# Performance work log

Hardware: AMD Instinct MI355X
Metric: run time of the kernel (lower is better)

The kernel has to match this reference:

```python
import jax, jax.numpy as jnp
import numpy as np

INV_TEMP = 100.0


def setup_inputs() -> dict:
    key = jax.random.key(0)
    k1, k2, k3 = jax.random.split(key, 3)
    B, C, J, Hh, Wh = 64, 4, 17, 96, 96
    heatmaps = jax.random.normal(k1, (B * C, J, Hh, Wh), dtype=jnp.float32)
    projection_matrices = jax.random.normal(k2, (B, C, 3, 4), dtype=jnp.float32)
    confidences = jax.random.uniform(k3, (B, C, J), dtype=jnp.float32)
    return {
        "heatmaps": heatmaps,
        "projection_matrices": projection_matrices,
        "confidences": confidences,
        "H_img": 384,
        "W_img": 384,
    }


def _softargmax(heatmaps):
    # heatmaps: (B*C, J, Hh, Wh) -> keypoints (B*C, J, 2) as (x, y)
    bc, J, Hh, Wh = heatmaps.shape
    hm = jax.nn.softmax((heatmaps * INV_TEMP).reshape(bc, J, Hh * Wh), axis=-1)
    hm = hm.reshape(bc, J, Hh, Wh)
    xs = jnp.arange(Wh, dtype=hm.dtype)
    ys = jnp.arange(Hh, dtype=hm.dtype)
    kx = jnp.einsum('bjhw,w->bj', hm, xs)  # x = width index (grid c=0)
    ky = jnp.einsum('bjhw,h->bj', hm, ys)  # y = height index (grid c=1)
    return jnp.stack([kx, ky], axis=-1)


def _dlt(P, kp2d, conf):
    # P: (B,C,3,4), kp2d: (B,C,J,2), conf: (B,C,J) -> (B,J,3)
    B, C, J = kp2d.shape[:3]
    # A[b,c,j,i,:] = P[b,c,2,:]*kp2d[b,c,j,i] - P[b,c,i,:], scaled by conf
    A = (P[:, :, None, 2:3, :] * kp2d[:, :, :, :, None]
         - P[:, :, None, :2, :]) * conf[:, :, :, None, None]  # (B,C,J,2,4)
    A = A.transpose(0, 2, 1, 3, 4).reshape(B, J, 2 * C, 4)
    _, _, Vh = jnp.linalg.svd(A, full_matrices=False)  # Vh: (B,J,4,4)
    homo = Vh[..., 3, :]  # smallest right singular vector, (B,J,4)
    return homo[..., :3] / homo[..., 3:4]


def reference(heatmaps, projection_matrices, confidences, H_img, W_img):
    B, C = projection_matrices.shape[:2]
    bc, J, Hh, Wh = heatmaps.shape
    kp = _softargmax(heatmaps)  # (B*C, J, 2)
    # faithful (quirky) rescale: x *= H/Hh, y *= W/Wh as in original code
    scale = jnp.array([H_img / Hh, W_img / Wh], dtype=kp.dtype)
    kp = (kp * scale).reshape(B, C, J, 2)
    return _dlt(projection_matrices, kp, confidences)
```

## Files before the change

kernel.cpp:

```cpp
#include <hip/hip_runtime.h>

#define B_NUM 64
#define C_NUM 4
#define J_NUM 17
#define HH 96
#define WW 96
#define HWSZ (HH * WW)

__device__ __forceinline__ float waveMax(float v) {
#pragma unroll
  for (int o = 32; o > 0; o >>= 1) v = fmaxf(v, __shfl_xor(v, o));
  return v;
}
__device__ __forceinline__ float waveSum(float v) {
#pragma unroll
  for (int o = 32; o > 0; o >>= 1) v += __shfl_xor(v, o);
  return v;
}

__global__ __launch_bounds__(256, 1) void triang_fused_k(
    const float* __restrict__ hm, const float* __restrict__ P,
    const float* __restrict__ conf, const int* __restrict__ Hp,
    const int* __restrict__ Wp, float* __restrict__ out) {
  const int bj = blockIdx.x;
  const int b = bj / J_NUM;
  const int j = bj - b * J_NUM;
  const int t = threadIdx.x;
  const int cam = t >> 6;
  const int lane = t & 63;
  const int r = (b * C_NUM + cam) * J_NUM + j;
  const float4* row = (const float4*)(hm + (size_t)r * HWSZ);

  float4 v[36];
  float m = -3.4e38f;
#pragma unroll
  for (int k = 0; k < 36; ++k) {
    v[k] = row[k * 64 + lane];
    m = fmaxf(m, fmaxf(fmaxf(v[k].x, v[k].y), fmaxf(v[k].z, v[k].w)));
  }
  m = waveMax(m);
  const float M100 = 100.0f * m;

  float se = 0.f, sx = 0.f, sy = 0.f;
#pragma unroll
  for (int k = 0; k < 36; ++k) {
    const int base = k * 256 + lane * 4;
    const float e0 = __expf(fmaf(100.f, v[k].x, -M100));
    const float e1 = __expf(fmaf(100.f, v[k].y, -M100));
    const float e2 = __expf(fmaf(100.f, v[k].z, -M100));
    const float e3 = __expf(fmaf(100.f, v[k].w, -M100));
    const int h = base / WW;
    const int w0 = base - h * WW;
    const float esum = (e0 + e1) + (e2 + e3);
    se += esum;
    sy += esum * (float)h;
    sx += e0 * (float)w0 + e1 * (float)(w0 + 1) + e2 * (float)(w0 + 2) +
          e3 * (float)(w0 + 3);
  }
  se = waveSum(se);
  sx = waveSum(sx);
  sy = waveSum(sy);

  __shared__ float skp[C_NUM][2];
  if (lane == 0) {
    const float scx = (float)Hp[0] / (float)HH;
    const float scy = (float)Wp[0] / (float)WW;
    skp[cam][0] = sx / se * scx;
    skp[cam][1] = sy / se * scy;
  }
  __syncthreads();
  if (t != 0) return;

  double M4[4][4];
#pragma unroll
  for (int a = 0; a < 4; ++a)
#pragma unroll
    for (int bb = 0; bb < 4; ++bb) M4[a][bb] = 0.0;

#pragma unroll
  for (int c = 0; c < C_NUM; ++c) {
    const float* Pm = P + ((size_t)(b * C_NUM + c)) * 12;
    const float cf = conf[(b * C_NUM + c) * J_NUM + j];
    const double x = (double)skp[c][0];
    const double y = (double)skp[c][1];
    double row0[4], row1[4];
#pragma unroll
    for (int l = 0; l < 4; ++l) {
      const double p2 = (double)Pm[8 + l];
      row0[l] = (p2 * x - (double)Pm[l]) * (double)cf;
      row1[l] = (p2 * y - (double)Pm[4 + l]) * (double)cf;
    }
#pragma unroll
    for (int a = 0; a < 4; ++a)
#pragma unroll
      for (int bb = 0; bb < 4; ++bb)
        M4[a][bb] += row0[a] * row0[bb] + row1[a] * row1[bb];
  }

  double V[4][4];
#pragma unroll
  for (int a = 0; a < 4; ++a)
#pragma unroll
    for (int bb = 0; bb < 4; ++bb) V[a][bb] = (a == bb) ? 1.0 : 0.0;

  for (int sweep = 0; sweep < 8; ++sweep) {
#pragma unroll
    for (int p = 0; p < 3; ++p) {
#pragma unroll
      for (int q = p + 1; q < 4; ++q) {
        const double d = M4[p][q];
        if (fabs(d) < 1e-300) continue;
        const double a = M4[p][p], bq = M4[q][q];
        const double theta = (bq - a) / (2.0 * d);
        const double tt = (theta >= 0.0 ? 1.0 : -1.0) /
                          (fabs(theta) + sqrt(theta * theta + 1.0));
        const double cc = 1.0 / sqrt(tt * tt + 1.0);
        const double ss = tt * cc;
#pragma unroll
        for (int k = 0; k < 4; ++k) {
          if (k == p || k == q) continue;
          const double mkp = M4[k][p], mkq = M4[k][q];
          M4[k][p] = M4[p][k] = cc * mkp - ss * mkq;
          M4[k][q] = M4[q][k] = ss * mkp + cc * mkq;
        }
        M4[p][p] = a - tt * d;
        M4[q][q] = bq + tt * d;
        M4[p][q] = M4[q][p] = 0.0;
#pragma unroll
        for (int k = 0; k < 4; ++k) {
          const double vkp = V[k][p], vkq = V[k][q];
          V[k][p] = cc * vkp - ss * vkq;
          V[k][q] = ss * vkp + cc * vkq;
        }
      }
    }
  }

  int mi = 0;
  double mv = M4[0][0];
#pragma unroll
  for (int i = 1; i < 4; ++i)
    if (M4[i][i] < mv) { mv = M4[i][i]; mi = i; }
  const double h3 = V[3][mi];
  out[bj * 3 + 0] = (float)(V[0][mi] / h3);
  out[bj * 3 + 1] = (float)(V[1][mi] / h3);
  out[bj * 3 + 2] = (float)(V[2][mi] / h3);
}

extern "C" void kernel_launch(void* const* d_in, const int* in_sizes, int n_in,
                              void* d_out, int out_size, void* d_ws, size_t ws_size,
                              hipStream_t stream) {
  const float* hm = (const float*)d_in[0];
  const float* P = (const float*)d_in[1];
  const float* conf = (const float*)d_in[2];
  const int* Hp = (const int*)d_in[3];
  const int* Wp = (const int*)d_in[4];
  float* out = (float*)d_out;

  triang_fused_k<<<B_NUM * J_NUM, 256, 0, stream>>>(hm, P, conf, Hp, Wp, out);
}
```

Before: 260.9 us.

## Stream heatmap rows with online softmax and double-buffered nontemporal loads

Replaces the load-everything-then-reduce scheme (36 float4 registers per thread) with four chunks of nine float4 loads. The next chunk is prefetched while the current one is reduced with an online max/rescale softmax. This is meant to cut register pressure so occupancy can rise beyond one block, now that the min-blocks launch bound is dropped. It also overlaps loads with exp math, uses nontemporal loads, and uses exp2 with a folded constant. The cost is extra rescale exps per chunk and one extra cross-lane rescale before the wave sums.

```diff
diff --git a/kernel.cpp b/kernel.cpp
--- a/kernel.cpp
+++ b/kernel.cpp
@@ -6,6 +6,9 @@
 #define HH 96
 #define WW 96
 #define HWSZ (HH * WW)
+#define K100 144.26950408889634f
+
+typedef float f32x4 __attribute__((ext_vector_type(4)));
 
 __device__ __forceinline__ float waveMax(float v) {
 #pragma unroll
@@ -18,48 +21,63 @@
   return v;
 }
 
-__global__ __launch_bounds__(256, 1) void triang_fused_k(
+__global__ __launch_bounds__(256) void triang_k(
     const float* __restrict__ hm, const float* __restrict__ P,
     const float* __restrict__ conf, const int* __restrict__ Hp,
     const int* __restrict__ Wp, float* __restrict__ out) {
   const int bj = blockIdx.x;
   const int b = bj / J_NUM;
   const int j = bj - b * J_NUM;
-  const int t = threadIdx.x;
-  const int cam = t >> 6;
-  const int lane = t & 63;
+  const int cam = threadIdx.x >> 6;
+  const int lane = threadIdx.x & 63;
   const int r = (b * C_NUM + cam) * J_NUM + j;
-  const float4* row = (const float4*)(hm + (size_t)r * HWSZ);
+  const f32x4* row = (const f32x4*)(hm + (size_t)r * HWSZ);
 
-  float4 v[36];
-  float m = -3.4e38f;
+  float m = -3.4e38f, se = 0.f, sx = 0.f, sy = 0.f;
+  f32x4 cur[9], nxt[9];
 #pragma unroll
-  for (int k = 0; k < 36; ++k) {
-    v[k] = row[k * 64 + lane];
-    m = fmaxf(m, fmaxf(fmaxf(v[k].x, v[k].y), fmaxf(v[k].z, v[k].w)));
+  for (int i = 0; i < 9; ++i)
+    cur[i] = __builtin_nontemporal_load(row + i * 64 + lane);
+
+#pragma unroll
+  for (int bb = 0; bb < 4; ++bb) {
+    if (bb < 3) {
+#pragma unroll
+      for (int i = 0; i < 9; ++i)
+        nxt[i] = __builtin_nontemporal_load(row + (bb + 1) * 576 + i * 64 + lane);
+    }
+    float c = -3.4e38f;
+#pragma unroll
+    for (int i = 0; i < 9; ++i)
+      c = fmaxf(c, fmaxf(fmaxf(cur[i][0], cur[i][1]), fmaxf(cur[i][2], cur[i][3])));
+    const float mn = fmaxf(m, c);
+    const float f = exp2f(K100 * (m - mn));
+    m = mn;
+    se *= f; sx *= f; sy *= f;
+    const float a = -K100 * mn;
+#pragma unroll
+    for (int i = 0; i < 9; ++i) {
+      const int flat = (bb * 9 + i) * 256 + lane * 4;
+      const int h = flat / WW;
+      const int w0 = flat - h * WW;
+      const float e0 = exp2f(fmaf(K100, cur[i][0], a));
+      const float e1 = exp2f(fmaf(K100, cur[i][1], a));
+      const float e2 = exp2f(fmaf(K100, cur[i][2], a));
+      const float e3 = exp2f(fmaf(K100, cur[i][3], a));
+      const float esum = (e0 + e1) + (e2 + e3);
+      se += esum;
+      sy = fmaf(esum, (float)h, sy);
+      sx += fmaf(esum, (float)w0, fmaf(2.f, e2, fmaf(3.f, e3, e1)));
+    }
+#pragma unroll
+    for (int i = 0; i < 9; ++i) cur[i] = nxt[i];
   }
-  m = waveMax(m);
-  const float M100 = 100.0f * m;
 
-  float se = 0.f, sx = 0.f, sy = 0.f;
-#pragma unroll
-  for (int k = 0; k < 36; ++k) {
-    const int base = k * 256 + lane * 4;
-    const float e0 = __expf(fmaf(100.f, v[k].x, -M100));
-    const float e1 = __expf(fmaf(100.f, v[k].y, -M100));
-    const float e2 = __expf(fmaf(100.f, v[k].z, -M100));
-    const float e3 = __expf(fmaf(100.f, v[k].w, -M100));
-    const int h = base / WW;
-    const int w0 = base - h * WW;
-    const float esum = (e0 + e1) + (e2 + e3);
-    se += esum;
-    sy += esum * (float)h;
-    sx += e0 * (float)w0 + e1 * (float)(w0 + 1) + e2 * (float)(w0 + 2) +
-          e3 * (float)(w0 + 3);
-  }
-  se = waveSum(se);
-  sx = waveSum(sx);
-  sy = waveSum(sy);
+  const float M = waveMax(m);
+  const float fw = exp2f(K100 * (m - M));
+  se = waveSum(se * fw);
+  sx = waveSum(sx * fw);
+  sy = waveSum(sy * fw);
 
   __shared__ float skp[C_NUM][2];
   if (lane == 0) {
@@ -69,13 +87,13 @@
     skp[cam][1] = sy / se * scy;
   }
   __syncthreads();
-  if (t != 0) return;
+  if (threadIdx.x != 0) return;
 
   double M4[4][4];
 #pragma unroll
   for (int a = 0; a < 4; ++a)
 #pragma unroll
-    for (int bb = 0; bb < 4; ++bb) M4[a][bb] = 0.0;
+    for (int q = 0; q < 4; ++q) M4[a][q] = 0.0;
 
 #pragma unroll
   for (int c = 0; c < C_NUM; ++c) {
@@ -93,15 +111,15 @@
 #pragma unroll
     for (int a = 0; a < 4; ++a)
 #pragma unroll
-      for (int bb = 0; bb < 4; ++bb)
-        M4[a][bb] += row0[a] * row0[bb] + row1[a] * row1[bb];
+      for (int q = 0; q < 4; ++q)
+        M4[a][q] += row0[a] * row0[q] + row1[a] * row1[q];
   }
 
   double V[4][4];
 #pragma unroll
   for (int a = 0; a < 4; ++a)
 #pragma unroll
-    for (int bb = 0; bb < 4; ++bb) V[a][bb] = (a == bb) ? 1.0 : 0.0;
+    for (int q = 0; q < 4; ++q) V[a][q] = (a == q) ? 1.0 : 0.0;
 
   for (int sweep = 0; sweep < 8; ++sweep) {
 #pragma unroll
@@ -157,5 +175,5 @@
   const int* Wp = (const int*)d_in[4];
   float* out = (float*)d_out;
 
-  triang_fused_k<<<B_NUM * J_NUM, 256, 0, stream>>>(hm, P, conf, Hp, Wp, out);
+  triang_k<<<B_NUM * J_NUM, 256, 0, stream>>>(hm, P, conf, Hp, Wp, out);
 }
```

New measurement: 242.3 us. -7.2%, faster.
